# Kernel tuning notes

Measured on AMD Instinct MI355X. Metric: run time of the kernel, lower is better.

Reference implementation:

```python
import jax, jax.numpy as jnp
import numpy as np

DEPTH = 8                 # tree depth -> 2^DEPTH leaves
INPUT_SIZE = 128
NB_CLASSES = 10
T = 65536                 # number of states in the trajectory (batched)
N_NODES = (1 << DEPTH) - 1   # 255 internal nodes (BFS order)
N_LEAVES = 1 << DEPTH        # 256 leaves
CLASS_REWARD = np.array([-1.0, -0.5, 0.0, 0.5, 1.0, 1.5, 2.0, 2.5, 3.0, 3.5], dtype=np.float32)


def setup_inputs() -> dict:
    key = jax.random.key(0)
    k_x, k_w, k_b, k_beta, k_leaf = jax.random.split(key, 5)
    x = jax.random.normal(k_x, (T, INPUT_SIZE), dtype=jnp.float32)
    # per-node Linear(input_size, 1): weight [N_NODES, INPUT_SIZE], bias [N_NODES]
    bound = 1.0 / np.sqrt(INPUT_SIZE)
    W = jax.random.uniform(k_w, (N_NODES, INPUT_SIZE), jnp.float32, -bound, bound)
    b = jax.random.uniform(k_b, (N_NODES,), jnp.float32, -bound, bound)
    beta = jax.random.uniform(k_beta, (N_NODES,), jnp.float32, 0.0, 1.0)   # torch.rand(1)
    leaf_dist = jax.random.uniform(k_leaf, (N_LEAVES, NB_CLASSES), jnp.float32, 0.0, 1.0)
    class_reward = jnp.asarray(CLASS_REWARD)
    return {"x": x, "W": W, "b": b, "beta": beta,
            "leaf_dist": leaf_dist, "class_reward": class_reward}


def reference(x, W, b, beta, leaf_dist, class_reward):
    # Gate prob at every internal node (BFS order): sigmoid(beta * (x @ w + b))
    # [T, N_NODES]
    p = jax.nn.sigmoid(beta[None, :] * (x @ W.T + b[None, :]))
    Tn = x.shape[0]
    depth = int(np.log2(p.shape[1] + 1))
    # Level-wise path-prob propagation: mu starts at root = 1.
    mu = jnp.ones((Tn, 1), dtype=x.dtype)
    offset = 0
    for d in range(depth):
        n = 1 << d
        p_lvl = p[:, offset:offset + n]                       # [T, n]
        # child[2i] gets p (left), child[2i+1] gets (1-p) (right)
        mu = (mu[:, :, None] * jnp.stack([p_lvl, 1.0 - p_lvl], axis=-1)).reshape(Tn, 2 * n)
        offset += n
    # Leaf class distributions and scalar reward per leaf
    Q = jax.nn.softmax(leaf_dist, axis=1)                     # [L, C]
    r = Q @ class_reward                                      # [L]
    # traj reward = sum over states and leaves of path_prob * leaf_reward
    return jnp.sum(mu @ r)
```

## Files before the change

### kernel.cpp

```cpp
#include <hip/hip_runtime.h>
#include <hip/hip_bf16.h>

#define NIN      128
#define NCLS     10
#define NNODES   255
#define TSAMP    65536

#define MBLK     64
#define NBLOCKS  (TSAMP / MBLK)
#define LPITCH   72

typedef short bf16x8 __attribute__((ext_vector_type(8)));
typedef short short4v __attribute__((ext_vector_type(4)));
typedef float f32x4  __attribute__((ext_vector_type(4)));

#define WS_BB  65280
#define WS_RD  66304
#define WS_R1  66816

__device__ __forceinline__ short f2b(float f) {
    return __builtin_bit_cast(short, __float2bfloat16(f));
}
__device__ __forceinline__ float b2f(short h) {
    return __builtin_bit_cast(float, ((unsigned)(unsigned short)h) << 16);
}
__device__ __forceinline__ bf16x8 mk8(float4 a, float4 b) {
    bf16x8 r;
    r[0] = f2b(a.x); r[1] = f2b(a.y); r[2] = f2b(a.z); r[3] = f2b(a.w);
    r[4] = f2b(b.x); r[5] = f2b(b.y); r[6] = f2b(b.z); r[7] = f2b(b.w);
    return r;
}

extern "C" __global__ void __launch_bounds__(128)
sdt_prep(const float* __restrict__ W, const float* __restrict__ b,
         const float* __restrict__ beta, const float* __restrict__ leaf_dist,
         const float* __restrict__ cr, char* __restrict__ ws) {
    short* Wbf = (short*)ws;
    float* bb  = (float*)(ws + WS_BB);
    float* rd  = (float*)(ws + WS_RD);
    float* r1  = (float*)(ws + WS_R1);
    const int n = blockIdx.x;
    const int t = threadIdx.x;
    if (n < NNODES) {
        const float be = beta[n];
        Wbf[n * NIN + t] = f2b(W[n * NIN + t] * be);
        if (t == 0) bb[n] = be * b[n];
    } else {
        float rv[2];
        #pragma unroll
        for (int h = 0; h < 2; ++h) {
            const float* ld = leaf_dist + (size_t)(2 * t + h) * NCLS;
            float mx = -1e30f;
            float v[NCLS];
            #pragma unroll
            for (int c = 0; c < NCLS; ++c) { v[c] = ld[c]; mx = fmaxf(mx, v[c]); }
            float s = 0.f, d = 0.f;
            #pragma unroll
            for (int c = 0; c < NCLS; ++c) { float e = __expf(v[c] - mx); s += e; d += e * cr[c]; }
            rv[h] = __fdividef(d, s);
        }
        rd[t] = rv[0] - rv[1];
        r1[t] = rv[1];
    }
}

extern "C" __global__ void __launch_bounds__(256, 4)
sdt_main(const float* __restrict__ x, const char* __restrict__ ws,
         float* __restrict__ out) {
    __shared__ short Lg[256 * LPITCH];
    __shared__ float bbS[256];
    __shared__ float rdS[128];
    __shared__ float r1S[128];
    __shared__ float v2S[4 * 64];
    __shared__ float red[8];

    const short* Wbf  = (const short*)ws;
    const float* g_bb = (const float*)(ws + WS_BB);
    const float* g_rd = (const float*)(ws + WS_RD);
    const float* g_r1 = (const float*)(ws + WS_R1);

    const int tid  = threadIdx.x;
    const int lane = tid & 63;
    const int w    = tid >> 6;

    bbS[tid] = (tid < NNODES) ? g_bb[tid] : 0.f;
    if (tid < 128) { rdS[tid] = g_rd[tid]; r1S[tid] = g_r1[tid]; }

    const int r16 = lane & 15;
    const int kg  = lane >> 4;
    const int m0  = blockIdx.x * MBLK;
    const int n0  = w * 64;

    f32x4 acc[4][4];
    #pragma unroll
    for (int i = 0; i < 4; ++i)
        #pragma unroll
        for (int j = 0; j < 4; ++j) acc[i][j] = (f32x4){0.f, 0.f, 0.f, 0.f};

    const float4* ap = (const float4*)(x + (size_t)(m0 + r16) * NIN + kg * 8);
    int nidx[4];
    #pragma unroll
    for (int nf = 0; nf < 4; ++nf) {
        int nn = n0 + nf * 16 + r16;
        nidx[nf] = (nn > 254) ? 254 : nn;
    }

    #pragma unroll
    for (int ks = 0; ks < 4; ++ks) {
        bf16x8 af[4], bfr[4];
        #pragma unroll
        for (int mf = 0; mf < 4; ++mf)
            af[mf] = mk8(ap[mf * 512 + ks * 8], ap[mf * 512 + ks * 8 + 1]);
        #pragma unroll
        for (int nf = 0; nf < 4; ++nf)
            bfr[nf] = *(const bf16x8*)(Wbf + nidx[nf] * NIN + ks * 32 + kg * 8);
        #pragma unroll
        for (int mf = 0; mf < 4; ++mf)
            #pragma unroll
            for (int nf = 0; nf < 4; ++nf)
                acc[mf][nf] = __builtin_amdgcn_mfma_f32_16x16x32_bf16(
                    af[mf], bfr[nf], acc[mf][nf], 0, 0, 0);
    }

    #pragma unroll
    for (int mf = 0; mf < 4; ++mf) {
        #pragma unroll
        for (int nf = 0; nf < 4; ++nf) {
            const int node = n0 + nf * 16 + r16;
            const int nd   = (node > 254) ? 254 : node;
            const int sl   = mf * 16 + kg * 4;
            short4v hv;
            hv[0] = f2b(acc[mf][nf][0]); hv[1] = f2b(acc[mf][nf][1]);
            hv[2] = f2b(acc[mf][nf][2]); hv[3] = f2b(acc[mf][nf][3]);
            *(short4v*)&Lg[nd * LPITCH + sl] = hv;
        }
    }
    __syncthreads();

    const int s = lane;
    const int g = w;

    auto SIG = [&](int node, int smp) -> float {
        float t = b2f(Lg[node * LPITCH + smp]) + bbS[node];
        return __fdividef(1.f, 1.f + __expf(-t));
    };

    float v7[32];
    #pragma unroll
    for (int i = 0; i < 32; ++i) {
        float p = SIG(127 + 32 * g + i, s);
        v7[i] = fmaf(p, rdS[32 * g + i], r1S[32 * g + i]);
    }
    float v6[16];
    #pragma unroll
    for (int i = 0; i < 16; ++i) {
        float p = SIG(63 + 16 * g + i, s);
        v6[i] = fmaf(p, v7[2 * i] - v7[2 * i + 1], v7[2 * i + 1]);
    }
    float v5[8];
    #pragma unroll
    for (int i = 0; i < 8; ++i) {
        float p = SIG(31 + 8 * g + i, s);
        v5[i] = fmaf(p, v6[2 * i] - v6[2 * i + 1], v6[2 * i + 1]);
    }
    float v4[4];
    #pragma unroll
    for (int i = 0; i < 4; ++i) {
        float p = SIG(15 + 4 * g + i, s);
        v4[i] = fmaf(p, v5[2 * i] - v5[2 * i + 1], v5[2 * i + 1]);
    }
    float v3[2];
    #pragma unroll
    for (int i = 0; i < 2; ++i) {
        float p = SIG(7 + 2 * g + i, s);
        v3[i] = fmaf(p, v4[2 * i] - v4[2 * i + 1], v4[2 * i + 1]);
    }
    {
        float p = SIG(3 + g, s);
        v2S[g * 64 + s] = fmaf(p, v3[0] - v3[1], v3[1]);
    }
    __syncthreads();

    if (tid < 64) {
        float p0 = SIG(0, tid);
        float p1 = SIG(1, tid);
        float p2 = SIG(2, tid);
        float L  = fmaf(p1, v2S[0 * 64 + tid] - v2S[1 * 64 + tid], v2S[1 * 64 + tid]);
        float R  = fmaf(p2, v2S[2 * 64 + tid] - v2S[3 * 64 + tid], v2S[3 * 64 + tid]);
        float val = fmaf(p0, L - R, R);
        #pragma unroll
        for (int off = 32; off > 0; off >>= 1) val += __shfl_down(val, off);
        if (tid == 0) atomicAdd(out, val);
    }
    (void)red;
}

extern "C" void kernel_launch(void* const* d_in, const int* in_sizes, int n_in,
                              void* d_out, int out_size, void* d_ws, size_t ws_size,
                              hipStream_t stream) {
    const float* x            = (const float*)d_in[0];
    const float* W            = (const float*)d_in[1];
    const float* b            = (const float*)d_in[2];
    const float* beta         = (const float*)d_in[3];
    const float* leaf_dist    = (const float*)d_in[4];
    const float* class_reward = (const float*)d_in[5];
    float* out = (float*)d_out;

    hipMemsetAsync(d_out, 0, sizeof(float), stream);

    sdt_prep<<<256, 128, 0, stream>>>(W, b, beta, leaf_dist, class_reward,
                                      (char*)d_ws);
    sdt_main<<<NBLOCKS, 256, 0, stream>>>(x, (const char*)d_ws, out);
}
```

Baseline: 118.6 us.

## Use single-wave blocks of 16 samples with shuffle-based final tree levels

Restructures the main kernel so each block is one wavefront handling 16 samples against all 255 nodes, instead of four waves handling 64 samples. The logit tile in shared memory shrinks and uses an XOR permutation of node indices instead of padding, and the last tree levels are combined with lane shuffles instead of a second barrier and shared buffer. LOG2E is folded into the prescaled weights so the sigmoid can use exp2f. The cost is four times as many blocks, each reloading the full bf16 weight matrix from global/L2, and more atomics on the output.

```diff
diff --git a/kernel.cpp b/kernel.cpp
--- a/kernel.cpp
+++ b/kernel.cpp
@@ -1,22 +1,24 @@
 #include <hip/hip_runtime.h>
 #include <hip/hip_bf16.h>
+#include <math.h>
 
 #define NIN      128
 #define NCLS     10
 #define NNODES   255
 #define TSAMP    65536
 
-#define MBLK     64
+#define MBLK     16
 #define NBLOCKS  (TSAMP / MBLK)
-#define LPITCH   72
-
-typedef short bf16x8 __attribute__((ext_vector_type(8)));
+
+typedef short bf16x8  __attribute__((ext_vector_type(8)));
 typedef short short4v __attribute__((ext_vector_type(4)));
-typedef float f32x4  __attribute__((ext_vector_type(4)));
+typedef float f32x4   __attribute__((ext_vector_type(4)));
 
 #define WS_BB  65280
 #define WS_RD  66304
 #define WS_R1  66816
+
+#define LOG2E  1.44269504088896f
 
 __device__ __forceinline__ short f2b(float f) {
     return __builtin_bit_cast(short, __float2bfloat16(f));
@@ -30,6 +32,7 @@
     r[4] = f2b(b.x); r[5] = f2b(b.y); r[6] = f2b(b.z); r[7] = f2b(b.w);
     return r;
 }
+__device__ __forceinline__ int perm(int n) { return n ^ ((n >> 5) & 3); }
 
 extern "C" __global__ void __launch_bounds__(128)
 sdt_prep(const float* __restrict__ W, const float* __restrict__ b,
@@ -42,7 +45,7 @@
     const int n = blockIdx.x;
     const int t = threadIdx.x;
     if (n < NNODES) {
-        const float be = beta[n];
+        const float be = beta[n] * LOG2E;
         Wbf[n * NIN + t] = f2b(W[n * NIN + t] * be);
         if (t == 0) bb[n] = be * b[n];
     } else {
@@ -50,8 +53,7 @@
         #pragma unroll
         for (int h = 0; h < 2; ++h) {
             const float* ld = leaf_dist + (size_t)(2 * t + h) * NCLS;
-            float mx = -1e30f;
-            float v[NCLS];
+            float mx = -1e30f, v[NCLS];
             #pragma unroll
             for (int c = 0; c < NCLS; ++c) { v[c] = ld[c]; mx = fmaxf(mx, v[c]); }
             float s = 0.f, d = 0.f;
@@ -64,85 +66,66 @@
     }
 }
 
-extern "C" __global__ void __launch_bounds__(256, 4)
+extern "C" __global__ void __launch_bounds__(64, 4)
 sdt_main(const float* __restrict__ x, const char* __restrict__ ws,
          float* __restrict__ out) {
-    __shared__ short Lg[256 * LPITCH];
+    __shared__ short Lg[256 * 16];
     __shared__ float bbS[256];
     __shared__ float rdS[128];
     __shared__ float r1S[128];
-    __shared__ float v2S[4 * 64];
-    __shared__ float red[8];
 
     const short* Wbf  = (const short*)ws;
     const float* g_bb = (const float*)(ws + WS_BB);
     const float* g_rd = (const float*)(ws + WS_RD);
     const float* g_r1 = (const float*)(ws + WS_R1);
 
-    const int tid  = threadIdx.x;
-    const int lane = tid & 63;
-    const int w    = tid >> 6;
-
-    bbS[tid] = (tid < NNODES) ? g_bb[tid] : 0.f;
-    if (tid < 128) { rdS[tid] = g_rd[tid]; r1S[tid] = g_r1[tid]; }
-
-    const int r16 = lane & 15;
-    const int kg  = lane >> 4;
-    const int m0  = blockIdx.x * MBLK;
-    const int n0  = w * 64;
-
-    f32x4 acc[4][4];
-    #pragma unroll
-    for (int i = 0; i < 4; ++i)
+    const int tid = threadIdx.x;
+    const int r16 = tid & 15;
+    const int kg  = tid >> 4;
+
+    ((float4*)bbS)[tid] = ((const float4*)g_bb)[tid];
+    if (tid < 32) ((float4*)rdS)[tid] = ((const float4*)g_rd)[tid];
+    else          ((float4*)r1S)[tid - 32] = ((const float4*)g_r1)[tid - 32];
+
+    const int m0 = blockIdx.x * MBLK;
+    const float4* ap = (const float4*)(x + (size_t)(m0 + r16) * NIN + kg * 8);
+
+    bf16x8 af[4];
+    #pragma unroll
+    for (int ks = 0; ks < 4; ++ks) af[ks] = mk8(ap[ks * 8], ap[ks * 8 + 1]);
+
+    f32x4 acc[16];
+    #pragma unroll
+    for (int i = 0; i < 16; ++i) acc[i] = (f32x4){0.f, 0.f, 0.f, 0.f};
+
+    #pragma unroll 4
+    for (int nf = 0; nf < 16; ++nf) {
+        int node = nf * 16 + r16;
+        int nd   = (node > 254) ? 254 : node;
+        const bf16x8* bp = (const bf16x8*)(Wbf + (size_t)nd * NIN);
         #pragma unroll
-        for (int j = 0; j < 4; ++j) acc[i][j] = (f32x4){0.f, 0.f, 0.f, 0.f};
-
-    const float4* ap = (const float4*)(x + (size_t)(m0 + r16) * NIN + kg * 8);
-    int nidx[4];
-    #pragma unroll
-    for (int nf = 0; nf < 4; ++nf) {
-        int nn = n0 + nf * 16 + r16;
-        nidx[nf] = (nn > 254) ? 254 : nn;
-    }
-
-    #pragma unroll
-    for (int ks = 0; ks < 4; ++ks) {
-        bf16x8 af[4], bfr[4];
-        #pragma unroll
-        for (int mf = 0; mf < 4; ++mf)
-            af[mf] = mk8(ap[mf * 512 + ks * 8], ap[mf * 512 + ks * 8 + 1]);
-        #pragma unroll
-        for (int nf = 0; nf < 4; ++nf)
-            bfr[nf] = *(const bf16x8*)(Wbf + nidx[nf] * NIN + ks * 32 + kg * 8);
-        #pragma unroll
-        for (int mf = 0; mf < 4; ++mf)
-            #pragma unroll
-            for (int nf = 0; nf < 4; ++nf)
-                acc[mf][nf] = __builtin_amdgcn_mfma_f32_16x16x32_bf16(
-                    af[mf], bfr[nf], acc[mf][nf], 0, 0, 0);
-    }
-
-    #pragma unroll
-    for (int mf = 0; mf < 4; ++mf) {
-        #pragma unroll
-        for (int nf = 0; nf < 4; ++nf) {
-            const int node = n0 + nf * 16 + r16;
-            const int nd   = (node > 254) ? 254 : node;
-            const int sl   = mf * 16 + kg * 4;
-            short4v hv;
-            hv[0] = f2b(acc[mf][nf][0]); hv[1] = f2b(acc[mf][nf][1]);
-            hv[2] = f2b(acc[mf][nf][2]); hv[3] = f2b(acc[mf][nf][3]);
-            *(short4v*)&Lg[nd * LPITCH + sl] = hv;
-        }
+        for (int ks = 0; ks < 4; ++ks)
+            acc[nf] = __builtin_amdgcn_mfma_f32_16x16x32_bf16(
+                af[ks], bp[kg + ks * 4], acc[nf], 0, 0, 0);
+    }
+
+    #pragma unroll
+    for (int nf = 0; nf < 16; ++nf) {
+        int node = nf * 16 + r16;
+        int nd   = (node > 254) ? 254 : node;
+        short4v hv;
+        hv[0] = f2b(acc[nf][0]); hv[1] = f2b(acc[nf][1]);
+        hv[2] = f2b(acc[nf][2]); hv[3] = f2b(acc[nf][3]);
+        *(short4v*)&Lg[perm(nd) * 16 + kg * 4] = hv;
     }
     __syncthreads();
 
-    const int s = lane;
-    const int g = w;
+    const int s = tid & 15;
+    const int g = tid >> 4;
 
     auto SIG = [&](int node, int smp) -> float {
-        float t = b2f(Lg[node * LPITCH + smp]) + bbS[node];
-        return __fdividef(1.f, 1.f + __expf(-t));
+        float t = b2f(Lg[perm(node) * 16 + smp]) + bbS[node];
+        return __fdividef(1.f, 1.f + exp2f(-t));
     };
 
     float v7[32];
@@ -175,24 +158,27 @@
         float p = SIG(7 + 2 * g + i, s);
         v3[i] = fmaf(p, v4[2 * i] - v4[2 * i + 1], v4[2 * i + 1]);
     }
+    float v2;
     {
         float p = SIG(3 + g, s);
-        v2S[g * 64 + s] = fmaf(p, v3[0] - v3[1], v3[1]);
-    }
-    __syncthreads();
-
-    if (tid < 64) {
-        float p0 = SIG(0, tid);
-        float p1 = SIG(1, tid);
-        float p2 = SIG(2, tid);
-        float L  = fmaf(p1, v2S[0 * 64 + tid] - v2S[1 * 64 + tid], v2S[1 * 64 + tid]);
-        float R  = fmaf(p2, v2S[2 * 64 + tid] - v2S[3 * 64 + tid], v2S[3 * 64 + tid]);
-        float val = fmaf(p0, L - R, R);
-        #pragma unroll
-        for (int off = 32; off > 0; off >>= 1) val += __shfl_down(val, off);
-        if (tid == 0) atomicAdd(out, val);
-    }
-    (void)red;
+        v2 = fmaf(p, v3[0] - v3[1], v3[1]);
+    }
+
+    float a0 = __shfl(v2, s);
+    float a1 = __shfl(v2, s + 16);
+    float a2 = __shfl(v2, s + 32);
+    float a3 = __shfl(v2, s + 48);
+    float p0 = SIG(0, s);
+    float p1 = SIG(1, s);
+    float p2 = SIG(2, s);
+    float L  = fmaf(p1, a0 - a1, a1);
+    float R  = fmaf(p2, a2 - a3, a3);
+    float val = fmaf(p0, L - R, R);
+    if (g != 0) val = 0.f;
+
+    #pragma unroll
+    for (int off = 32; off > 0; off >>= 1) val += __shfl_down(val, off);
+    if (tid == 0) atomicAdd(out, val);
 }
 
 extern "C" void kernel_launch(void* const* d_in, const int* in_sizes, int n_in,
@@ -210,5 +196,5 @@
 
     sdt_prep<<<256, 128, 0, stream>>>(W, b, beta, leaf_dist, class_reward,
                                       (char*)d_ws);
-    sdt_main<<<NBLOCKS, 256, 0, stream>>>(x, (const char*)d_ws, out);
-}
+    sdt_main<<<NBLOCKS, 64, 0, stream>>>(x, (const char*)d_ws, out);
+}
```

New measurement: 182.9 us. +54.3%, slower.
